# Optimization experiments

Measured on AMD Instinct MI355X. Metric: run time of the kernel, lower is better.

## Reference

```python
import jax, jax.numpy as jnp
from jax import lax
import numpy as np

B = 2048
N = 10  # wires on q_device0
C64 = jnp.complex64

# fixed gate matrices (qubit ordering matches wire-list order)
S_ = jnp.array([[1, 0], [0, 1j]], C64)
T_ = jnp.array([[1, 0], [0, np.exp(1j * np.pi / 4)]], C64)
SX_ = 0.5 * jnp.array([[1 + 1j, 1 - 1j], [1 - 1j, 1 + 1j]], C64)
Y_ = jnp.array([[0, -1j], [1j, 0]], C64)
CNOT_ = jnp.array([[1, 0, 0, 0], [0, 1, 0, 0], [0, 0, 0, 1], [0, 0, 1, 0]], C64)
CZ_ = jnp.diag(jnp.array([1, 1, 1, -1], C64))
CY_ = jnp.array([[1, 0, 0, 0], [0, 1, 0, 0], [0, 0, 0, -1j], [0, 0, 1j, 0]], C64)
SWAP_ = jnp.array([[1, 0, 0, 0], [0, 0, 1, 0], [0, 1, 0, 0], [0, 0, 0, 1]], C64)
_cs = np.eye(8); _cs[[5, 6]] = _cs[[6, 5]]  # CSWAP: |101> <-> |110>
CSWAP_ = jnp.array(_cs, C64)
_tf = np.eye(8); _tf[[6, 7]] = _tf[[7, 6]]  # Toffoli: |110> <-> |111>
TOFF_ = jnp.array(_tf, C64)

# parametrized single-qubit gate builders; t scalar -> [2,2], t [B] -> [B,2,2]
def _rx(t):
    c = jnp.cos(t / 2).astype(C64)
    s = -1j * jnp.sin(t / 2).astype(C64)
    return jnp.stack([jnp.stack([c, s], -1), jnp.stack([s, c], -1)], -2)

def _ry(t):
    c = jnp.cos(t / 2).astype(C64)
    s = jnp.sin(t / 2).astype(C64)
    return jnp.stack([jnp.stack([c, -s], -1), jnp.stack([s, c], -1)], -2)

def _rz(t):
    a = jnp.exp(-0.5j * t.astype(C64))
    b = jnp.exp(0.5j * t.astype(C64))
    z = jnp.zeros_like(a)
    return jnp.stack([jnp.stack([a, z], -1), jnp.stack([z, b], -1)], -2)

def _phase(t):
    e = jnp.exp(1j * t.astype(C64))
    o = jnp.ones_like(e)
    z = jnp.zeros_like(e)
    return jnp.stack([jnp.stack([o, z], -1), jnp.stack([z, e], -1)], -2)

def _rot(phi, th, om):  # RZ(om) RY(th) RZ(phi), pennylane/torchquantum convention
    c = jnp.cos(th / 2).astype(C64)
    s = jnp.sin(th / 2).astype(C64)
    p = phi.astype(C64); w = om.astype(C64)
    m00 = jnp.exp(-0.5j * (p + w)) * c
    m01 = -jnp.exp(0.5j * (p - w)) * s
    m10 = jnp.exp(-0.5j * (p - w)) * s
    m11 = jnp.exp(0.5j * (p + w)) * c
    return jnp.stack([jnp.stack([m00, m01], -1), jnp.stack([m10, m11], -1)], -2)

def _apply1(psi, U, w):  # psi: [B]+(2,)*N, U: [2,2] or [B,2,2]
    s = jnp.moveaxis(psi, w + 1, 1)
    if U.ndim == 2:
        s = jnp.einsum('ij,bj...->bi...', U, s)
    else:
        s = jnp.einsum('bij,bj...->bi...', U, s)
    return jnp.moveaxis(s, 1, w + 1)

def _applyk(psi, U, wires):  # fixed k-qubit gate, U: [2^k, 2^k]
    k = len(wires)
    axes = tuple(w + 1 for w in wires)
    s = jnp.moveaxis(psi, axes, tuple(range(1, k + 1)))
    sh = s.shape
    s = s.reshape((sh[0], 2 ** k) + sh[k + 1:])
    s = jnp.einsum('ij,bj...->bi...', U, s)
    return jnp.moveaxis(s.reshape(sh), tuple(range(1, k + 1)), axes)

def _forward(x, conv1_w, conv1_b, conv2_w, conv2_b, fc1_w, fc1_b, fc2_w, fc2_b,
             theta0, theta_rz, theta_ps, rot_p):
    dn = ('NCHW', 'OIHW', 'NCHW')
    h = lax.conv_general_dilated(x, conv1_w, (1, 1), 'VALID', dimension_numbers=dn)
    h = jax.nn.relu(h + conv1_b[None, :, None, None])
    h = lax.conv_general_dilated(h, conv2_w, (1, 1), 'VALID', dimension_numbers=dn)
    h = jax.nn.relu(h + conv2_b[None, :, None, None])
    h = lax.reduce_window(h, -jnp.inf, lax.max, (1, 1, 2, 2), (1, 1, 2, 2), 'VALID')
    h = h.reshape(h.shape[0], -1)  # [B, 9216], dropout = identity (eval)
    h = jax.nn.relu(h @ fc1_w.T + fc1_b)
    a = jax.nn.sigmoid(h @ fc2_w.T + fc2_b) * (2.0 * np.pi)  # angles [B, 10]
    bsz = a.shape[0]
    psi = jnp.zeros((bsz, 2 ** N), C64).at[:, 0].set(1.0).reshape((bsz,) + (2,) * N)
    trz = jnp.reshape(theta_rz, ())
    tps = jnp.reshape(theta_ps, ())
    for k in range(N):                      # TrainableRxAll
        psi = _apply1(psi, _rx(theta0[k]), k)
    for k in range(N):                      # RxAll with input angles
        psi = _apply1(psi, _rx(a[:, k]), k)
    psi = _apply1(psi, _rx(a[:, 1]), 1)
    psi = _apply1(psi, _rx(jnp.asarray(-np.pi / 4, jnp.float32)), 5)  # q_layer2 fixed
    psi = _apply1(psi, _ry(a[:, 2]), 2)
    psi = _apply1(psi, _rz(a[:, 3]), 3)
    psi = _apply1(psi, S_, 4)
    psi = _apply1(psi, T_, 5)
    psi = _apply1(psi, _rz(trz), 6)         # q_layer3
    psi = _apply1(psi, SX_, 7)
    # (q_device1 ops on a separate 3-wire device do not affect the output)
    psi = _applyk(psi, CZ_, (0, 5))
    psi = _applyk(psi, CNOT_, (0, 5))
    psi = _applyk(psi, CY_, (0, 5))
    psi = _applyk(psi, CY_, (3, 8))         # q_layer4
    psi = _applyk(psi, SWAP_, (2, 3))
    psi = _applyk(psi, CSWAP_, (4, 5, 6))
    psi = _applyk(psi, TOFF_, (8, 5, 0))    # q_layer5
    psi = _apply1(psi, _phase(tps), 8)      # q_layer6
    psi = _apply1(psi, _phase(a[:, 7]), 7)
    psi = _apply1(psi, _rot(rot_p[0], rot_p[1], rot_p[2]), 4)  # q_layer7
    psi = _apply1(psi, _rot(a[:, 6], a[:, 7], a[:, 8]), 5)
    axes = tuple(range(1, N + 1))
    evs = [jnp.real(jnp.sum(jnp.conj(psi) * _apply1(psi, Y_, k), axis=axes))
           for k in range(N)]
    ev = jnp.stack(evs, -1)                 # [B, 10] <Y_k>
    return jax.nn.log_softmax(ev, axis=1)


def setup_inputs() -> dict:
    key = jax.random.key(0)
    ks = jax.random.split(key, 13)
    return {
        'x': jax.random.normal(ks[0], (B, 1, 28, 28), jnp.float32),
        'conv1_w': jax.random.normal(ks[1], (32, 1, 3, 3), jnp.float32) * 0.2,
        'conv1_b': jnp.zeros((32,), jnp.float32),
        'conv2_w': jax.random.normal(ks[2], (64, 32, 3, 3), jnp.float32) * 0.05,
        'conv2_b': jnp.zeros((64,), jnp.float32),
        'fc1_w': jax.random.normal(ks[3], (128, 9216), jnp.float32) * 0.01,
        'fc1_b': jnp.zeros((128,), jnp.float32),
        'fc2_w': jax.random.normal(ks[4], (10, 128), jnp.float32) * 0.1,
        'fc2_b': jnp.zeros((10,), jnp.float32),
        'theta0': jax.random.normal(ks[5], (10,), jnp.float32),
        'theta_rz': jax.random.normal(ks[6], (1,), jnp.float32),
        'theta_ps': jax.random.normal(ks[7], (1,), jnp.float32),
        'rot_p': jax.random.normal(ks[8], (3,), jnp.float32),
    }


def reference(x, conv1_w, conv1_b, conv2_w, conv2_b, fc1_w, fc1_b, fc2_w, fc2_b,
              theta0, theta_rz, theta_ps, rot_p):
    return _forward(x, conv1_w, conv1_b, conv2_w, conv2_b, fc1_w, fc1_b, fc2_w, fc2_b,
                    theta0, theta_rz, theta_ps, rot_p)
```

## Files before the change

kernel.cpp:

```cpp
#include <hip/hip_runtime.h>
#include <math.h>

typedef short short8 __attribute__((ext_vector_type(8)));
typedef float f32x4 __attribute__((ext_vector_type(4)));
typedef float f32x16 __attribute__((ext_vector_type(16)));

#define GLB_CP(p) ((const __attribute__((address_space(1))) void*)(p))
#define LDS_CP(p) ((__attribute__((address_space(3))) void*)(p))

__device__ __forceinline__ float2 cmul(float2 a, float2 b) {
    return make_float2(a.x * b.x - a.y * b.y, a.x * b.y + a.y * b.x);
}

__device__ __forceinline__ ushort f2bf(float f) {
    uint u = __float_as_uint(f);
    uint r = (u + 0x7FFFu + ((u >> 16) & 1u)) >> 16;
    return (ushort)r;
}

__global__ __launch_bounds__(256) void prep_kernel(
    const float* __restrict__ c2w, const float* __restrict__ f1w,
    ushort* __restrict__ wt2, ushort* __restrict__ wf1)
{
    int i = blockIdx.x * 256 + threadIdx.x;
    if (i < 18432) {
        int icl = i & 7;
        int t = i >> 3;
        int oc = t & 63;
        int t2 = t >> 6;
        int icg = t2 & 3;
        int tap = t2 >> 2;
        int ic = icg * 8 + icl;
        wt2[i] = f2bf(c2w[(oc * 32 + ic) * 9 + tap]);
    } else if (i < 18432 + 1179648) {
        int j = i - 18432;
        wf1[j] = f2bf(f1w[j]);
    }
}

__global__ __launch_bounds__(256) void conv1_kernel(
    const float* __restrict__ x, const float* __restrict__ w1,
    const float* __restrict__ b1, ushort* __restrict__ h1b)
{
    __shared__ float wl[288];
    __shared__ float bl[32];
    int tid = threadIdx.x;
    for (int e = tid; e < 288; e += 256) wl[e] = w1[e];
    if (tid < 32) bl[tid] = b1[tid];
    __syncthreads();
    int e = blockIdx.x * 256 + tid;
    int icg = e & 3;
    int t = e >> 2;
    int pix = t % 676;
    int b = t / 676;
    int y = pix / 26, xc = pix % 26;
    const float* xp = x + b * 784 + y * 28 + xc;
    float in9[9];
#pragma unroll
    for (int ky = 0; ky < 3; ++ky)
#pragma unroll
        for (int kx = 0; kx < 3; ++kx) in9[ky * 3 + kx] = xp[ky * 28 + kx];
    short8 outv;
#pragma unroll
    for (int o = 0; o < 8; ++o) {
        int oc = icg * 8 + o;
        float acc = bl[oc];
#pragma unroll
        for (int k = 0; k < 9; ++k) acc = fmaf(in9[k], wl[oc * 9 + k], acc);
        outv[o] = (short)f2bf(fmaxf(acc, 0.f));
    }
    *(short8*)&h1b[((b * 4 + icg) * 676 + pix) * 8] = outv;
}

#define EPILOG(ACC0, ACC1, RX, RY)                                                         \
    {                                                                                      \
        int pcolb = (RX) * 4 + 2 * hi;                                                     \
        _Pragma("unroll")                                                                  \
        for (int q = 0; q < 2; ++q) {                                                      \
            int prow = (RY) * 2 + q;                                                       \
            int bs = 8 * q;                                                                \
            float m00 = fmaxf(fmaxf(ACC0[bs], ACC0[bs + 1]), fmaxf(ACC0[bs + 4], ACC0[bs + 5])); \
            float m01 = fmaxf(fmaxf(ACC0[bs + 2], ACC0[bs + 3]), fmaxf(ACC0[bs + 6], ACC0[bs + 7])); \
            uint pk0 = (uint)f2bf(fmaxf(m00 + bias0, 0.f)) | ((uint)f2bf(fmaxf(m01 + bias0, 0.f)) << 16); \
            *(uint*)&pout[lo * 144 + prow * 12 + pcolb] = pk0;                             \
            float m10 = fmaxf(fmaxf(ACC1[bs], ACC1[bs + 1]), fmaxf(ACC1[bs + 4], ACC1[bs + 5])); \
            float m11 = fmaxf(fmaxf(ACC1[bs + 2], ACC1[bs + 3]), fmaxf(ACC1[bs + 6], ACC1[bs + 7])); \
            uint pk1 = (uint)f2bf(fmaxf(m10 + bias1, 0.f)) | ((uint)f2bf(fmaxf(m11 + bias1, 0.f)) << 16); \
            *(uint*)&pout[(lo + 32) * 144 + prow * 12 + pcolb] = pk1;                      \
        }                                                                                  \
    }

__global__ __launch_bounds__(384, 2) void conv2_persist(
    const ushort* __restrict__ h1b, const ushort* __restrict__ wt2,
    const float* __restrict__ c2b, ushort* __restrict__ pooled)
{
    __shared__ __attribute__((aligned(16))) ushort wt_lds[18432];
    __shared__ __attribute__((aligned(16))) ushort in_lds[2][22016];
    int cu = blockIdx.x;
    int tid = threadIdx.x;
    int wave = tid >> 6;
    int lane = tid & 63;
    int lo = lane & 31;
    int hi = lane >> 5;

    for (int c = wave; c < 36; c += 6) {
        const ushort* src = wt2 + (size_t)(c * 64 + lane) * 8;
        __builtin_amdgcn_global_load_lds(GLB_CP(src), LDS_CP(wt_lds + c * 512), 16, 0, 0);
    }
    {
        const ushort* base = h1b + (size_t)(cu * 8) * 21632;
        for (int c = wave; c < 43; c += 6) {
            int e = c * 64 + lane;
            if (e > 2703) e = 2703;
            __builtin_amdgcn_global_load_lds(GLB_CP(base + (size_t)e * 8),
                                             LDS_CP(in_lds[0] + c * 512), 16, 0, 0);
        }
    }
    float bias0 = c2b[lo];
    float bias1 = c2b[lo + 32];
    __syncthreads();

    int pb[3];
#pragma unroll
    for (int i = 0; i < 3; ++i) {
        int r = wave + 6 * i;
        int rx = r % 3, ry = r / 3;
        int xcoord = rx * 8 + (lo & 7);
        int ycoord = ry * 4 + (lo >> 3);
        pb[i] = ycoord * 26 + xcoord;
    }
    int rx0 = wave % 3, ry0 = wave / 3;
    int rx1 = (wave + 6) % 3, ry1 = (wave + 6) / 3;
    int rx2 = (wave + 12) % 3, ry2 = (wave + 12) / 3;

    for (int j = 0; j < 8; ++j) {
        if (j < 7) {
            const ushort* base = h1b + (size_t)(cu * 8 + j + 1) * 21632;
            ushort* dst = in_lds[(j + 1) & 1];
            for (int c = wave; c < 43; c += 6) {
                int e = c * 64 + lane;
                if (e > 2703) e = 2703;
                __builtin_amdgcn_global_load_lds(GLB_CP(base + (size_t)e * 8),
                                                 LDS_CP(dst + c * 512), 16, 0, 0);
            }
        }

        const ushort* ib = in_lds[j & 1];
        f32x16 aA0 = (f32x16)0.f, aA1 = (f32x16)0.f;
        f32x16 aB0 = (f32x16)0.f, aB1 = (f32x16)0.f;
        f32x16 aC0 = (f32x16)0.f, aC1 = (f32x16)0.f;

#pragma unroll
        for (int tap = 0; tap < 9; ++tap) {
            int off = (tap / 3) * 26 + (tap % 3);
#pragma unroll
            for (int ks = 0; ks < 2; ++ks) {
                const ushort* wp = &wt_lds[((tap * 4 + ks * 2 + hi) * 64) * 8];
                short8 a0 = *(const short8*)(wp + lo * 8);
                short8 a1 = *(const short8*)(wp + (32 + lo) * 8);
                const ushort* ip = &ib[((ks * 2 + hi) * 676 + off) * 8];
                short8 b0 = *(const short8*)(ip + pb[0] * 8);
                short8 b1 = *(const short8*)(ip + pb[1] * 8);
                short8 b2 = *(const short8*)(ip + pb[2] * 8);
                aA0 = __builtin_amdgcn_mfma_f32_32x32x16_bf16(b0, a0, aA0, 0, 0, 0);
                aA1 = __builtin_amdgcn_mfma_f32_32x32x16_bf16(b0, a1, aA1, 0, 0, 0);
                aB0 = __builtin_amdgcn_mfma_f32_32x32x16_bf16(b1, a0, aB0, 0, 0, 0);
                aB1 = __builtin_amdgcn_mfma_f32_32x32x16_bf16(b1, a1, aB1, 0, 0, 0);
                aC0 = __builtin_amdgcn_mfma_f32_32x32x16_bf16(b2, a0, aC0, 0, 0, 0);
                aC1 = __builtin_amdgcn_mfma_f32_32x32x16_bf16(b2, a1, aC1, 0, 0, 0);
            }
        }

        ushort* pout = pooled + (size_t)(cu * 8 + j) * 9216;
        EPILOG(aA0, aA1, rx0, ry0)
        EPILOG(aB0, aB1, rx1, ry1)
        EPILOG(aC0, aC1, rx2, ry2)
        __syncthreads();
    }
}

__global__ __launch_bounds__(256) void fc1_mfma(
    const ushort* __restrict__ pooled, const ushort* __restrict__ wf1,
    float* __restrict__ part)
{
    int bx = blockIdx.x, by = blockIdx.y;
    int tid = threadIdx.x;
    int wid = tid >> 6, lane = tid & 63;
    int lo = lane & 15, hi = lane >> 4;
    int m0 = bx * 32;
    int kb = by * 2304;

    f32x4 acc[2][2];
#pragma unroll
    for (int mt = 0; mt < 2; ++mt)
#pragma unroll
        for (int j = 0; j < 2; ++j) acc[mt][j] = (f32x4)0.f;

    const ushort* arow0 = pooled + (size_t)(m0 + lo) * 9216 + kb + hi * 8;
    const ushort* arow1 = arow0 + 16 * 9216;
    const ushort* brow0 = wf1 + (size_t)(wid * 32 + lo) * 9216 + kb + hi * 8;
    const ushort* brow1 = brow0 + 16 * 9216;

    for (int kt = 0; kt < 72; ++kt) {
        short8 a0 = *(const short8*)(arow0 + kt * 32);
        short8 a1 = *(const short8*)(arow1 + kt * 32);
        short8 b0 = *(const short8*)(brow0 + kt * 32);
        short8 b1 = *(const short8*)(brow1 + kt * 32);
        acc[0][0] = __builtin_amdgcn_mfma_f32_16x16x32_bf16(a0, b0, acc[0][0], 0, 0, 0);
        acc[1][0] = __builtin_amdgcn_mfma_f32_16x16x32_bf16(a1, b0, acc[1][0], 0, 0, 0);
        acc[0][1] = __builtin_amdgcn_mfma_f32_16x16x32_bf16(a0, b1, acc[0][1], 0, 0, 0);
        acc[1][1] = __builtin_amdgcn_mfma_f32_16x16x32_bf16(a1, b1, acc[1][1], 0, 0, 0);
    }
    float* pp = part + (size_t)by * 262144;
#pragma unroll
    for (int mt = 0; mt < 2; ++mt)
#pragma unroll
        for (int j = 0; j < 2; ++j)
#pragma unroll
            for (int r = 0; r < 4; ++r)
                pp[(m0 + mt * 16 + hi * 4 + r) * 128 + wid * 32 + j * 16 + lo] = acc[mt][j][r];
}

__global__ __launch_bounds__(256) void fc1_reduce_kernel(
    const float* __restrict__ part, const float* __restrict__ bias,
    float* __restrict__ outp)
{
    int idx = blockIdx.x * 256 + threadIdx.x;
    float s = 0.f;
#pragma unroll
    for (int ks = 0; ks < 4; ++ks) s += part[ks * 262144 + idx];
    outp[idx] = fmaxf(s + bias[idx & 127], 0.f);
}

__global__ __launch_bounds__(256) void fc2_kernel(
    const float* __restrict__ h, const float* __restrict__ w,
    const float* __restrict__ bias, float* __restrict__ ang)
{
    int idx = blockIdx.x * 256 + threadIdx.x;
    if (idx >= 20480) return;
    int b = idx / 10, n = idx % 10;
    const float* hp = h + b * 128;
    const float* wp = w + n * 128;
    float s = bias[n];
    for (int k = 0; k < 128; ++k) s = fmaf(hp[k], wp[k], s);
    ang[idx] = 6.28318530718f / (1.f + expf(-s));
}

__device__ __forceinline__ void apply_rot(float2* s, int p, float phi, float th,
                                          float om, int tid)
{
    float c, sn; sincosf(0.5f * th, &sn, &c);
    float A = 0.5f * (phi + om), Bv = 0.5f * (phi - om);
    float cA, sA; sincosf(A, &sA, &cA);
    float cB, sB; sincosf(Bv, &sB, &cB);
    float2 m00 = make_float2(cA * c, -sA * c);
    float2 m01 = make_float2(-cB * sn, -sB * sn);
    float2 m10 = make_float2(cB * sn, -sB * sn);
    float2 m11 = make_float2(cA * c, sA * c);
    for (int q = tid; q < 512; q += 256) {
        int i0 = ((q >> p) << (p + 1)) | (q & ((1 << p) - 1));
        int i1 = i0 | (1 << p);
        float2 aa = s[i0], bb = s[i1];
        s[i0] = make_float2(m00.x * aa.x - m00.y * aa.y + m01.x * bb.x - m01.y * bb.y,
                            m00.x * aa.y + m00.y * aa.x + m01.x * bb.y + m01.y * bb.x);
        s[i1] = make_float2(m10.x * aa.x - m10.y * aa.y + m11.x * bb.x - m11.y * bb.y,
                            m10.x * aa.y + m10.y * aa.x + m11.x * bb.y + m11.y * bb.x);
    }
}

__global__ __launch_bounds__(256) void quantum_kernel(
    const float* __restrict__ ang, const float* __restrict__ theta0,
    const float* __restrict__ theta_rz, const float* __restrict__ theta_ps,
    const float* __restrict__ rot_p, float* __restrict__ out)
{
    __shared__ float2 s[1024];
    __shared__ float red[40];
    int b = blockIdx.x;
    int tid = threadIdx.x;

    float a[10];
#pragma unroll
    for (int k = 0; k < 10; ++k) a[k] = ang[b * 10 + k];
    float th[10];
#pragma unroll
    for (int k = 0; k < 10; ++k) th[k] = theta0[k] + a[k];
    th[1] += a[1];
    th[5] -= 0.78539816339745f;

    float2 v[10][2];
#pragma unroll
    for (int k = 0; k < 10; ++k) {
        float c, sn; sincosf(0.5f * th[k], &sn, &c);
        v[k][0] = make_float2(c, 0.f);
        v[k][1] = make_float2(0.f, -sn);
    }
    { float c, sn; sincosf(0.5f * a[2], &sn, &c);
      float2 v0 = v[2][0], v1 = v[2][1];
      v[2][0] = make_float2(c * v0.x - sn * v1.x, c * v0.y - sn * v1.y);
      v[2][1] = make_float2(sn * v0.x + c * v1.x, sn * v0.y + c * v1.y); }
    { float c, sn; sincosf(0.5f * a[3], &sn, &c);
      v[3][0] = cmul(v[3][0], make_float2(c, -sn));
      v[3][1] = cmul(v[3][1], make_float2(c, sn)); }
    { float2 t = v[4][1]; v[4][1] = make_float2(-t.y, t.x); }
    { const float r = 0.70710678118655f;
      float2 t = v[5][1]; v[5][1] = make_float2(r * (t.x - t.y), r * (t.x + t.y)); }
    { float c, sn; sincosf(0.5f * theta_rz[0], &sn, &c);
      v[6][0] = cmul(v[6][0], make_float2(c, -sn));
      v[6][1] = cmul(v[6][1], make_float2(c, sn)); }
    { float2 p = v[7][0], q = v[7][1];
      v[7][0] = make_float2(0.5f * ((p.x - p.y) + (q.x + q.y)),
                            0.5f * ((p.x + p.y) + (q.y - q.x)));
      v[7][1] = make_float2(0.5f * ((p.x + p.y) + (q.x - q.y)),
                            0.5f * ((p.y - p.x) + (q.x + q.y))); }

    for (int i = tid; i < 1024; i += 256) {
        float2 c = ((i >> 9) & 1) ? v[0][1] : v[0][0];
#pragma unroll
        for (int k = 1; k < 10; ++k) {
            float2 vk = ((i >> (9 - k)) & 1) ? v[k][1] : v[k][0];
            c = cmul(c, vk);
        }
        s[i] = c;
    }
    __syncthreads();

    for (int i = tid; i < 1024; i += 256)
        if (((i >> 9) & 1) && ((i >> 4) & 1)) { s[i].x = -s[i].x; s[i].y = -s[i].y; }
    __syncthreads();
    { int j = tid;
      int i0 = 512 | ((j >> 4) << 5) | (j & 15);
      int i1 = i0 | 16;
      float2 t0 = s[i0], t1 = s[i1];
      s[i0] = t1; s[i1] = t0; }
    __syncthreads();
    { int j = tid;
      int i0 = 512 | ((j >> 4) << 5) | (j & 15);
      int i1 = i0 | 16;
      float2 t0 = s[i0], t1 = s[i1];
      s[i0] = make_float2(t1.y, -t1.x);
      s[i1] = make_float2(-t0.y, t0.x); }
    __syncthreads();
    { int j = tid;
      int i0 = (j & 1) | (((j >> 1) & 15) << 2) | (((j >> 5) & 7) << 7) | 64;
      int i1 = i0 | 2;
      float2 t0 = s[i0], t1 = s[i1];
      s[i0] = make_float2(t1.y, -t1.x);
      s[i1] = make_float2(-t0.y, t0.x); }
    __syncthreads();
    { int j = tid;
      int i0 = (j & 63) | 128 | (((j >> 6) & 3) << 8);
      int i1 = i0 ^ 0xC0;
      float2 t0 = s[i0], t1 = s[i1];
      s[i0] = t1; s[i1] = t0; }
    __syncthreads();
    if (tid < 128) {
      int j = tid;
      int i0 = (j & 7) | 16 | 32 | (((j >> 3) & 15) << 6);
      int i1 = i0 ^ 0x18;
      float2 t0 = s[i0], t1 = s[i1];
      s[i0] = t1; s[i1] = t0; }
    __syncthreads();
    if (tid < 128) {
      int j = tid;
      int i0 = (j & 1) | 2 | (((j >> 1) & 3) << 2) | 16 | (((j >> 3) & 15) << 5);
      int i1 = i0 | 512;
      float2 t0 = s[i0], t1 = s[i1];
      s[i0] = t1; s[i1] = t0; }
    __syncthreads();
    { float c1, s1; sincosf(theta_ps[0], &s1, &c1);
      float c2, s2; sincosf(a[7], &s2, &c2);
      float2 p1 = make_float2(c1, s1), p2 = make_float2(c2, s2);
      for (int i = tid; i < 1024; i += 256) {
          float2 t = s[i];
          if ((i >> 1) & 1) t = cmul(t, p1);
          if ((i >> 2) & 1) t = cmul(t, p2);
          s[i] = t;
      } }
    __syncthreads();
    apply_rot(s, 5, rot_p[0], rot_p[1], rot_p[2], tid);
    __syncthreads();
    apply_rot(s, 4, a[6], a[7], a[8], tid);
    __syncthreads();

    int wave = tid >> 6;
    for (int k = 0; k < 10; ++k) {
        int p = 9 - k;
        float part = 0.f;
        for (int q = tid; q < 512; q += 256) {
            int i0 = ((q >> p) << (p + 1)) | (q & ((1 << p) - 1));
            int i1 = i0 | (1 << p);
            float2 aa = s[i0], bb = s[i1];
            part += aa.x * bb.y - aa.y * bb.x;
        }
        part *= 2.f;
#pragma unroll
        for (int off = 32; off > 0; off >>= 1)
            part += __shfl_down(part, off, 64);
        if ((tid & 63) == 0) red[k * 4 + wave] = part;
    }
    __syncthreads();
    if (tid == 0) {
        float ev[10];
        float mx = -1e30f;
#pragma unroll
        for (int k = 0; k < 10; ++k) {
            ev[k] = red[k * 4] + red[k * 4 + 1] + red[k * 4 + 2] + red[k * 4 + 3];
            mx = fmaxf(mx, ev[k]);
        }
        float sum = 0.f;
#pragma unroll
        for (int k = 0; k < 10; ++k) sum += expf(ev[k] - mx);
        float lse = mx + logf(sum);
#pragma unroll
        for (int k = 0; k < 10; ++k) out[b * 10 + k] = ev[k] - lse;
    }
}

extern "C" void kernel_launch(void* const* d_in, const int* in_sizes, int n_in,
                              void* d_out, int out_size, void* d_ws, size_t ws_size,
                              hipStream_t stream)
{
    (void)in_sizes; (void)n_in; (void)out_size; (void)ws_size;
    const float* x    = (const float*)d_in[0];
    const float* c1w  = (const float*)d_in[1];
    const float* c1b  = (const float*)d_in[2];
    const float* c2w  = (const float*)d_in[3];
    const float* c2b  = (const float*)d_in[4];
    const float* f1w  = (const float*)d_in[5];
    const float* f1b  = (const float*)d_in[6];
    const float* f2w  = (const float*)d_in[7];
    const float* f2b  = (const float*)d_in[8];
    const float* th0  = (const float*)d_in[9];
    const float* trz  = (const float*)d_in[10];
    const float* tps  = (const float*)d_in[11];
    const float* rotp = (const float*)d_in[12];
    float* out = (float*)d_out;

    char* ws = (char*)d_ws;
    ushort* h1b    = (ushort*)(ws);
    ushort* pooled = (ushort*)(ws + 88604672);
    ushort* wt2    = (ushort*)(ws + 126353408);
    ushort* wf1    = (ushort*)(ws + 126390272);
    float*  part   = (float*)(ws + 128749568);
    float*  fc1o   = (float*)(ws + 132943872);
    float*  ang    = (float*)(ws + 133992448);

    prep_kernel<<<4680, 256, 0, stream>>>(c2w, f1w, wt2, wf1);
    conv1_kernel<<<21632, 256, 0, stream>>>(x, c1w, c1b, h1b);
    conv2_persist<<<256, 384, 0, stream>>>(h1b, wt2, c2b, pooled);
    fc1_mfma<<<dim3(64, 4), 256, 0, stream>>>(pooled, wf1, part);
    fc1_reduce_kernel<<<1024, 256, 0, stream>>>(part, f1b, fc1o);
    fc2_kernel<<<80, 256, 0, stream>>>(fc1o, f2w, f2b, ang);
    quantum_kernel<<<2048, 256, 0, stream>>>(ang, th0, trz, tps, rotp, out);
}
```

Baseline: 155.0 us.

## Fuse fc2 into per-sample quantum parameter precompute kernel

After: 185.6 us. +19.7%, slower.

```diff
diff --git a/kernel.cpp b/kernel.cpp
--- a/kernel.cpp
+++ b/kernel.cpp
@@ -232,55 +232,23 @@
     outp[idx] = fmaxf(s + bias[idx & 127], 0.f);
 }
 
-__global__ __launch_bounds__(256) void fc2_kernel(
-    const float* __restrict__ h, const float* __restrict__ w,
-    const float* __restrict__ bias, float* __restrict__ ang)
-{
-    int idx = blockIdx.x * 256 + threadIdx.x;
-    if (idx >= 20480) return;
-    int b = idx / 10, n = idx % 10;
-    const float* hp = h + b * 128;
-    const float* wp = w + n * 128;
-    float s = bias[n];
-    for (int k = 0; k < 128; ++k) s = fmaf(hp[k], wp[k], s);
-    ang[idx] = 6.28318530718f / (1.f + expf(-s));
-}
-
-__device__ __forceinline__ void apply_rot(float2* s, int p, float phi, float th,
-                                          float om, int tid)
-{
-    float c, sn; sincosf(0.5f * th, &sn, &c);
-    float A = 0.5f * (phi + om), Bv = 0.5f * (phi - om);
-    float cA, sA; sincosf(A, &sA, &cA);
-    float cB, sB; sincosf(Bv, &sB, &cB);
-    float2 m00 = make_float2(cA * c, -sA * c);
-    float2 m01 = make_float2(-cB * sn, -sB * sn);
-    float2 m10 = make_float2(cB * sn, -sB * sn);
-    float2 m11 = make_float2(cA * c, sA * c);
-    for (int q = tid; q < 512; q += 256) {
-        int i0 = ((q >> p) << (p + 1)) | (q & ((1 << p) - 1));
-        int i1 = i0 | (1 << p);
-        float2 aa = s[i0], bb = s[i1];
-        s[i0] = make_float2(m00.x * aa.x - m00.y * aa.y + m01.x * bb.x - m01.y * bb.y,
-                            m00.x * aa.y + m00.y * aa.x + m01.x * bb.y + m01.y * bb.x);
-        s[i1] = make_float2(m10.x * aa.x - m10.y * aa.y + m11.x * bb.x - m11.y * bb.y,
-                            m10.x * aa.y + m10.y * aa.x + m11.x * bb.y + m11.y * bb.x);
-    }
-}
-
-__global__ __launch_bounds__(256) void quantum_kernel(
-    const float* __restrict__ ang, const float* __restrict__ theta0,
+__global__ __launch_bounds__(256) void qprep_kernel(
+    const float* __restrict__ h, const float* __restrict__ f2w,
+    const float* __restrict__ f2b, const float* __restrict__ theta0,
     const float* __restrict__ theta_rz, const float* __restrict__ theta_ps,
-    const float* __restrict__ rot_p, float* __restrict__ out)
-{
-    __shared__ float2 s[1024];
-    __shared__ float red[40];
-    int b = blockIdx.x;
-    int tid = threadIdx.x;
-
+    const float* __restrict__ rot_p, float* __restrict__ params)
+{
+    int item = blockIdx.x * 256 + threadIdx.x;
+    if (item >= 2048) return;
+    const float* hp = h + (size_t)item * 128;
     float a[10];
 #pragma unroll
-    for (int k = 0; k < 10; ++k) a[k] = ang[b * 10 + k];
+    for (int n = 0; n < 10; ++n) {
+        const float* wp = f2w + n * 128;
+        float s = f2b[n];
+        for (int k = 0; k < 128; ++k) s = fmaf(hp[k], wp[k], s);
+        a[n] = 6.28318530718f / (1.f + expf(-s));
+    }
     float th[10];
 #pragma unroll
     for (int k = 0; k < 10; ++k) th[k] = theta0[k] + a[k];
@@ -313,6 +281,71 @@
       v[7][1] = make_float2(0.5f * ((p.x + p.y) + (q.x - q.y)),
                             0.5f * ((p.y - p.x) + (q.x + q.y))); }
 
+    float P[64];
+#pragma unroll
+    for (int k = 0; k < 10; ++k) {
+        P[k * 4 + 0] = v[k][0].x; P[k * 4 + 1] = v[k][0].y;
+        P[k * 4 + 2] = v[k][1].x; P[k * 4 + 3] = v[k][1].y;
+    }
+    { float c1, s1; sincosf(theta_ps[0], &s1, &c1); P[40] = c1; P[41] = s1; }
+    { float c2, s2; sincosf(a[7], &s2, &c2); P[42] = c2; P[43] = s2; }
+    {
+      float c, sn; sincosf(0.5f * rot_p[1], &sn, &c);
+      float A = 0.5f * (rot_p[0] + rot_p[2]), Bv = 0.5f * (rot_p[0] - rot_p[2]);
+      float cA, sA; sincosf(A, &sA, &cA);
+      float cB, sB; sincosf(Bv, &sB, &cB);
+      P[44] = cA * c;  P[45] = -sA * c;
+      P[46] = -cB * sn; P[47] = -sB * sn;
+      P[48] = cB * sn;  P[49] = -sB * sn;
+      P[50] = cA * c;  P[51] = sA * c; }
+    {
+      float c, sn; sincosf(0.5f * a[7], &sn, &c);
+      float A = 0.5f * (a[6] + a[8]), Bv = 0.5f * (a[6] - a[8]);
+      float cA, sA; sincosf(A, &sA, &cA);
+      float cB, sB; sincosf(Bv, &sB, &cB);
+      P[52] = cA * c;  P[53] = -sA * c;
+      P[54] = -cB * sn; P[55] = -sB * sn;
+      P[56] = cB * sn;  P[57] = -sB * sn;
+      P[58] = cA * c;  P[59] = sA * c; }
+    P[60] = 0.f; P[61] = 0.f; P[62] = 0.f; P[63] = 0.f;
+
+    float4* dst = (float4*)(params + (size_t)item * 64);
+#pragma unroll
+    for (int q = 0; q < 16; ++q)
+        dst[q] = make_float4(P[q * 4], P[q * 4 + 1], P[q * 4 + 2], P[q * 4 + 3]);
+}
+
+__device__ __forceinline__ void apply_rot2(float2* s, int p, float2 m00, float2 m01,
+                                           float2 m10, float2 m11, int tid)
+{
+    for (int q = tid; q < 512; q += 256) {
+        int i0 = ((q >> p) << (p + 1)) | (q & ((1 << p) - 1));
+        int i1 = i0 | (1 << p);
+        float2 aa = s[i0], bb = s[i1];
+        s[i0] = make_float2(m00.x * aa.x - m00.y * aa.y + m01.x * bb.x - m01.y * bb.y,
+                            m00.x * aa.y + m00.y * aa.x + m01.x * bb.y + m01.y * bb.x);
+        s[i1] = make_float2(m10.x * aa.x - m10.y * aa.y + m11.x * bb.x - m11.y * bb.y,
+                            m10.x * aa.y + m10.y * aa.x + m11.x * bb.y + m11.y * bb.x);
+    }
+}
+
+__global__ __launch_bounds__(256) void quantum_kernel(
+    const float* __restrict__ params, float* __restrict__ out)
+{
+    __shared__ float2 s[1024];
+    __shared__ float red[40];
+    int b = blockIdx.x;
+    int tid = threadIdx.x;
+    const float* P = params + (size_t)b * 64;
+
+    float2 v[10][2];
+#pragma unroll
+    for (int k = 0; k < 10; ++k) {
+        float4 t = *(const float4*)(P + k * 4);
+        v[k][0] = make_float2(t.x, t.y);
+        v[k][1] = make_float2(t.z, t.w);
+    }
+
     for (int i = tid; i < 1024; i += 256) {
         float2 c = ((i >> 9) & 1) ? v[0][1] : v[0][0];
 #pragma unroll
@@ -367,9 +400,7 @@
       float2 t0 = s[i0], t1 = s[i1];
       s[i0] = t1; s[i1] = t0; }
     __syncthreads();
-    { float c1, s1; sincosf(theta_ps[0], &s1, &c1);
-      float c2, s2; sincosf(a[7], &s2, &c2);
-      float2 p1 = make_float2(c1, s1), p2 = make_float2(c2, s2);
+    { float2 p1 = make_float2(P[40], P[41]), p2 = make_float2(P[42], P[43]);
       for (int i = tid; i < 1024; i += 256) {
           float2 t = s[i];
           if ((i >> 1) & 1) t = cmul(t, p1);
@@ -377,9 +408,11 @@
           s[i] = t;
       } }
     __syncthreads();
-    apply_rot(s, 5, rot_p[0], rot_p[1], rot_p[2], tid);
-    __syncthreads();
-    apply_rot(s, 4, a[6], a[7], a[8], tid);
+    apply_rot2(s, 5, make_float2(P[44], P[45]), make_float2(P[46], P[47]),
+               make_float2(P[48], P[49]), make_float2(P[50], P[51]), tid);
+    __syncthreads();
+    apply_rot2(s, 4, make_float2(P[52], P[53]), make_float2(P[54], P[55]),
+               make_float2(P[56], P[57]), make_float2(P[58], P[59]), tid);
     __syncthreads();
 
     int wave = tid >> 6;
@@ -443,13 +476,13 @@
     ushort* wf1    = (ushort*)(ws + 126390272);
     float*  part   = (float*)(ws + 128749568);
     float*  fc1o   = (float*)(ws + 132943872);
-    float*  ang    = (float*)(ws + 133992448);
+    float*  params = (float*)(ws + 133992448);
 
     prep_kernel<<<4680, 256, 0, stream>>>(c2w, f1w, wt2, wf1);
     conv1_kernel<<<21632, 256, 0, stream>>>(x, c1w, c1b, h1b);
     conv2_persist<<<256, 384, 0, stream>>>(h1b, wt2, c2b, pooled);
     fc1_mfma<<<dim3(64, 4), 256, 0, stream>>>(pooled, wf1, part);
     fc1_reduce_kernel<<<1024, 256, 0, stream>>>(part, f1b, fc1o);
-    fc2_kernel<<<80, 256, 0, stream>>>(fc1o, f2w, f2b, ang);
-    quantum_kernel<<<2048, 256, 0, stream>>>(ang, th0, trz, tps, rotp, out);
-}
+    qprep_kernel<<<8, 256, 0, stream>>>(fc1o, f2w, f2b, th0, trz, tps, rotp, params);
+    quantum_kernel<<<2048, 256, 0, stream>>>(params, out);
+}
```

## Fold fixed gates into product-state factors and share per-batch gate parameters via LDS

Applied to the files above, without the earlier changes.

After: 151.2 us. 2.5% less time.

```diff
diff --git a/kernel.cpp b/kernel.cpp
--- a/kernel.cpp
+++ b/kernel.cpp
@@ -246,17 +246,9 @@
     ang[idx] = 6.28318530718f / (1.f + expf(-s));
 }
 
-__device__ __forceinline__ void apply_rot(float2* s, int p, float phi, float th,
-                                          float om, int tid)
-{
-    float c, sn; sincosf(0.5f * th, &sn, &c);
-    float A = 0.5f * (phi + om), Bv = 0.5f * (phi - om);
-    float cA, sA; sincosf(A, &sA, &cA);
-    float cB, sB; sincosf(Bv, &sB, &cB);
-    float2 m00 = make_float2(cA * c, -sA * c);
-    float2 m01 = make_float2(-cB * sn, -sB * sn);
-    float2 m10 = make_float2(cB * sn, -sB * sn);
-    float2 m11 = make_float2(cA * c, sA * c);
+__device__ __forceinline__ void apply_rot2(float2* s, int p, float2 m00, float2 m01,
+                                           float2 m10, float2 m11, int tid)
+{
     for (int q = tid; q < 512; q += 256) {
         int i0 = ((q >> p) << (p + 1)) | (q & ((1 << p) - 1));
         int i1 = i0 | (1 << p);
@@ -275,43 +267,75 @@
 {
     __shared__ float2 s[1024];
     __shared__ float red[40];
+    __shared__ float P[64];
     int b = blockIdx.x;
     int tid = threadIdx.x;
 
-    float a[10];
-#pragma unroll
-    for (int k = 0; k < 10; ++k) a[k] = ang[b * 10 + k];
-    float th[10];
-#pragma unroll
-    for (int k = 0; k < 10; ++k) th[k] = theta0[k] + a[k];
-    th[1] += a[1];
-    th[5] -= 0.78539816339745f;
+    if (tid < 13) {
+        if (tid < 10) {
+            int k = tid;
+            float ak = ang[b * 10 + k];
+            float th = theta0[k] + ak;
+            if (k == 1) th += ak;
+            if (k == 5) th -= 0.78539816339745f;
+            float c, sn; sincosf(0.5f * th, &sn, &c);
+            float2 v0 = make_float2(c, 0.f), v1 = make_float2(0.f, -sn);
+            if (k == 0) v1 = make_float2(-sn, 0.f);
+            if (k == 2) { float ca, sa; sincosf(0.5f * ak, &sa, &ca);
+                float2 n0 = make_float2(ca * v0.x - sa * v1.x, ca * v0.y - sa * v1.y);
+                float2 n1 = make_float2(sa * v0.x + ca * v1.x, sa * v0.y + ca * v1.y);
+                v0 = n0; v1 = n1; }
+            if (k == 3) { float ca, sa; sincosf(0.5f * ak, &sa, &ca);
+                v0 = cmul(v0, make_float2(ca, -sa));
+                v1 = cmul(v1, make_float2(ca, sa)); }
+            if (k == 4) { float2 t = v1; v1 = make_float2(-t.y, t.x); }
+            if (k == 5) { const float r = 0.70710678118655f;
+                float2 t = v1; v1 = make_float2(r * (t.x - t.y), r * (t.x + t.y)); }
+            if (k == 6) { float ca, sa; sincosf(0.5f * theta_rz[0], &sa, &ca);
+                v0 = cmul(v0, make_float2(ca, -sa));
+                v1 = cmul(v1, make_float2(ca, sa)); }
+            if (k == 7) { float2 p = v0, q = v1;
+                v0 = make_float2(0.5f * ((p.x - p.y) + (q.x + q.y)),
+                                 0.5f * ((p.x + p.y) + (q.y - q.x)));
+                v1 = make_float2(0.5f * ((p.x + p.y) + (q.x - q.y)),
+                                 0.5f * ((p.y - p.x) + (q.x + q.y)));
+                float c2, s2; sincosf(ak, &s2, &c2);
+                v1 = cmul(v1, make_float2(c2, s2)); }
+            P[k * 4 + 0] = v0.x; P[k * 4 + 1] = v0.y;
+            P[k * 4 + 2] = v1.x; P[k * 4 + 3] = v1.y;
+        } else if (tid == 10) {
+            float c1, s1; sincosf(theta_ps[0], &s1, &c1);
+            P[40] = c1; P[41] = s1;
+        } else if (tid == 11) {
+            float c, sn; sincosf(0.5f * rot_p[1], &sn, &c);
+            float A = 0.5f * (rot_p[0] + rot_p[2]), Bv = 0.5f * (rot_p[0] - rot_p[2]);
+            float cA, sA; sincosf(A, &sA, &cA);
+            float cB, sB; sincosf(Bv, &sB, &cB);
+            P[44] = cA * c;  P[45] = -sA * c;
+            P[46] = -cB * sn; P[47] = -sB * sn;
+            P[48] = cB * sn;  P[49] = -sB * sn;
+            P[50] = cA * c;  P[51] = sA * c;
+        } else {
+            float a6 = ang[b * 10 + 6], a7 = ang[b * 10 + 7], a8 = ang[b * 10 + 8];
+            float c, sn; sincosf(0.5f * a7, &sn, &c);
+            float A = 0.5f * (a6 + a8), Bv = 0.5f * (a6 - a8);
+            float cA, sA; sincosf(A, &sA, &cA);
+            float cB, sB; sincosf(Bv, &sB, &cB);
+            P[52] = cA * c;  P[53] = -sA * c;
+            P[54] = -cB * sn; P[55] = -sB * sn;
+            P[56] = cB * sn;  P[57] = -sB * sn;
+            P[58] = cA * c;  P[59] = sA * c;
+        }
+    }
+    __syncthreads();
 
     float2 v[10][2];
 #pragma unroll
     for (int k = 0; k < 10; ++k) {
-        float c, sn; sincosf(0.5f * th[k], &sn, &c);
-        v[k][0] = make_float2(c, 0.f);
-        v[k][1] = make_float2(0.f, -sn);
-    }
-    { float c, sn; sincosf(0.5f * a[2], &sn, &c);
-      float2 v0 = v[2][0], v1 = v[2][1];
-      v[2][0] = make_float2(c * v0.x - sn * v1.x, c * v0.y - sn * v1.y);
-      v[2][1] = make_float2(sn * v0.x + c * v1.x, sn * v0.y + c * v1.y); }
-    { float c, sn; sincosf(0.5f * a[3], &sn, &c);
-      v[3][0] = cmul(v[3][0], make_float2(c, -sn));
-      v[3][1] = cmul(v[3][1], make_float2(c, sn)); }
-    { float2 t = v[4][1]; v[4][1] = make_float2(-t.y, t.x); }
-    { const float r = 0.70710678118655f;
-      float2 t = v[5][1]; v[5][1] = make_float2(r * (t.x - t.y), r * (t.x + t.y)); }
-    { float c, sn; sincosf(0.5f * theta_rz[0], &sn, &c);
-      v[6][0] = cmul(v[6][0], make_float2(c, -sn));
-      v[6][1] = cmul(v[6][1], make_float2(c, sn)); }
-    { float2 p = v[7][0], q = v[7][1];
-      v[7][0] = make_float2(0.5f * ((p.x - p.y) + (q.x + q.y)),
-                            0.5f * ((p.x + p.y) + (q.y - q.x)));
-      v[7][1] = make_float2(0.5f * ((p.x + p.y) + (q.x - q.y)),
-                            0.5f * ((p.y - p.x) + (q.x + q.y))); }
+        int slot = (k == 2) ? 3 : (k == 3) ? 2 : k;
+        v[k][0] = make_float2(P[slot * 4], P[slot * 4 + 1]);
+        v[k][1] = make_float2(P[slot * 4 + 2], P[slot * 4 + 3]);
+    }
 
     for (int i = tid; i < 1024; i += 256) {
         float2 c = ((i >> 9) & 1) ? v[0][1] : v[0][0];
@@ -324,62 +348,39 @@
     }
     __syncthreads();
 
-    for (int i = tid; i < 1024; i += 256)
-        if (((i >> 9) & 1) && ((i >> 4) & 1)) { s[i].x = -s[i].x; s[i].y = -s[i].y; }
-    __syncthreads();
-    { int j = tid;
-      int i0 = 512 | ((j >> 4) << 5) | (j & 15);
-      int i1 = i0 | 16;
-      float2 t0 = s[i0], t1 = s[i1];
-      s[i0] = t1; s[i1] = t0; }
-    __syncthreads();
-    { int j = tid;
-      int i0 = 512 | ((j >> 4) << 5) | (j & 15);
-      int i1 = i0 | 16;
-      float2 t0 = s[i0], t1 = s[i1];
-      s[i0] = make_float2(t1.y, -t1.x);
-      s[i1] = make_float2(-t0.y, t0.x); }
-    __syncthreads();
-    { int j = tid;
-      int i0 = (j & 1) | (((j >> 1) & 15) << 2) | (((j >> 5) & 7) << 7) | 64;
-      int i1 = i0 | 2;
-      float2 t0 = s[i0], t1 = s[i1];
-      s[i0] = make_float2(t1.y, -t1.x);
-      s[i1] = make_float2(-t0.y, t0.x); }
-    __syncthreads();
-    { int j = tid;
-      int i0 = (j & 63) | 128 | (((j >> 6) & 3) << 8);
-      int i1 = i0 ^ 0xC0;
-      float2 t0 = s[i0], t1 = s[i1];
-      s[i0] = t1; s[i1] = t0; }
+    {
+        int j = tid;
+        float2 p1 = make_float2(P[40], P[41]);
+        int i0 = (j & 1) | (((j >> 1) & 31) << 2) | (((j >> 6) & 3) << 8) | 128;
+        int i1 = i0 | 2;
+        float2 t0 = s[i0], t1 = s[i1];
+        s[i0] = make_float2(t1.y, -t1.x);
+        s[i1] = cmul(make_float2(-t0.y, t0.x), p1);
+        int i2 = (j & 1) | 2 | (((j >> 1) & 31) << 2) | (((j >> 6) & 3) << 8);
+        s[i2] = cmul(s[i2], p1);
+    }
     __syncthreads();
     if (tid < 128) {
-      int j = tid;
-      int i0 = (j & 7) | 16 | 32 | (((j >> 3) & 15) << 6);
-      int i1 = i0 ^ 0x18;
-      float2 t0 = s[i0], t1 = s[i1];
-      s[i0] = t1; s[i1] = t0; }
+        int j = tid;
+        int i0 = (j & 7) | 16 | 32 | (((j >> 3) & 15) << 6);
+        int i1 = i0 ^ 0x18;
+        float2 t0 = s[i0], t1 = s[i1];
+        s[i0] = t1; s[i1] = t0;
+    }
     __syncthreads();
     if (tid < 128) {
-      int j = tid;
-      int i0 = (j & 1) | 2 | (((j >> 1) & 3) << 2) | 16 | (((j >> 3) & 15) << 5);
-      int i1 = i0 | 512;
-      float2 t0 = s[i0], t1 = s[i1];
-      s[i0] = t1; s[i1] = t0; }
-    __syncthreads();
-    { float c1, s1; sincosf(theta_ps[0], &s1, &c1);
-      float c2, s2; sincosf(a[7], &s2, &c2);
-      float2 p1 = make_float2(c1, s1), p2 = make_float2(c2, s2);
-      for (int i = tid; i < 1024; i += 256) {
-          float2 t = s[i];
-          if ((i >> 1) & 1) t = cmul(t, p1);
-          if ((i >> 2) & 1) t = cmul(t, p2);
-          s[i] = t;
-      } }
-    __syncthreads();
-    apply_rot(s, 5, rot_p[0], rot_p[1], rot_p[2], tid);
-    __syncthreads();
-    apply_rot(s, 4, a[6], a[7], a[8], tid);
+        int j = tid;
+        int i0 = (j & 1) | 2 | (((j >> 1) & 3) << 2) | 16 | (((j >> 3) & 15) << 5);
+        int i1 = i0 | 512;
+        float2 t0 = s[i0], t1 = s[i1];
+        s[i0] = t1; s[i1] = t0;
+    }
+    __syncthreads();
+    apply_rot2(s, 5, make_float2(P[44], P[45]), make_float2(P[46], P[47]),
+               make_float2(P[48], P[49]), make_float2(P[50], P[51]), tid);
+    __syncthreads();
+    apply_rot2(s, 4, make_float2(P[52], P[53]), make_float2(P[54], P[55]),
+               make_float2(P[56], P[57]), make_float2(P[58], P[59]), tid);
     __syncthreads();
 
     int wave = tid >> 6;
```
